# Optimization experiments

Measured on AMD Instinct MI355X. Metric: run time of the kernel, lower is better.

## Reference

```python
import jax, jax.numpy as jnp
import numpy as np

TEMPERATURE = 0.07
NORMALIZE = True
NEG_INF = -1e30


def setup_inputs() -> dict:
    key = jax.random.key(0)
    features = jax.random.normal(key, (8192, 512), dtype=jnp.float32)
    return {"features": features}


def reference(features):
    # features: [B, D]
    B = features.shape[0]
    if NORMALIZE:
        norm = jnp.linalg.norm(features, axis=1, keepdims=True)
        features = features / jnp.maximum(norm, 1e-12)
    # [B, B] similarity matrix
    sim = jnp.matmul(features, features.T) / TEMPERATURE

    # default SimCLR labels: arange(B//2) repeated twice -> pair (i, i + B//2)
    half = jnp.arange(B // 2, dtype=jnp.int32)
    labels = jnp.concatenate([half, half])
    eq = labels[None, :] == labels[:, None]          # [B, B]
    diag = jnp.eye(B, dtype=bool)
    mask_pos = eq & ~diag                            # positives per row

    # Original per-row CE: logits = cat(pos_sims, neg_sims) (= all j != i),
    # target index 0 = FIRST positive (lowest column index). Loss_i =
    # logsumexp_{j != i}(sim[i, j]) - sim[i, first_pos_i].
    sim_masked = jnp.where(diag, NEG_INF, sim)
    lse = jax.scipy.special.logsumexp(sim_masked, axis=1)   # [B]

    first_pos = jnp.argmax(mask_pos, axis=1)                 # first True per row
    pos_sim = jnp.take_along_axis(sim, first_pos[:, None], axis=1)[:, 0]

    has_pos = jnp.any(mask_pos, axis=1)
    losses = jnp.where(has_pos, lse - pos_sim, 0.0)
    count = jnp.maximum(jnp.sum(has_pos.astype(jnp.float32)), 1.0)
    return jnp.sum(losses) / count
```

## Files before the change

kernel.cpp:

```cpp
#include <hip/hip_runtime.h>
#include <hip/hip_bf16.h>
#include <stdint.h>

#define BATCH 8192
#define DIM   512
#define BM    256
#define BK    64
#define NT    (BATCH / BM)
#define NPAIR (NT * (NT + 1) / 2)

#define FEAT_SCALE 4.5398164f
#define LN2        0.69314718055994531f

typedef __attribute__((ext_vector_type(8))) short short8;
typedef __attribute__((ext_vector_type(4))) float f32x4;

__device__ __forceinline__ void gld_lds16(const void* g, void* l) {
  __builtin_amdgcn_global_load_lds(
      (__attribute__((address_space(1))) void*)(uintptr_t)g,
      (__attribute__((address_space(3))) void*)(uintptr_t)l,
      16, 0, 0);
}

__global__ __launch_bounds__(256) void normalize_bf16(
    const float* __restrict__ x, __hip_bfloat16* __restrict__ o,
    float* __restrict__ rowsum) {
  const int wv = threadIdx.x >> 6, lane = threadIdx.x & 63;
  const int row = blockIdx.x * 4 + wv;
  if (lane == 0) rowsum[row] = 0.0f;
  const float4* xr = (const float4*)(x + (size_t)row * DIM);
  const float4 v0 = xr[lane];
  const float4 v1 = xr[lane + 64];
  float ss = v0.x * v0.x + v0.y * v0.y + v0.z * v0.z + v0.w * v0.w +
             v1.x * v1.x + v1.y * v1.y + v1.z * v1.z + v1.w * v1.w;
#pragma unroll
  for (int m = 32; m > 0; m >>= 1) ss += __shfl_xor(ss, m, 64);
  const float inv = FEAT_SCALE / fmaxf(sqrtf(ss), 1e-12f);
  ushort4 p0, p1;
  p0.x = __bfloat16_as_ushort(__float2bfloat16(v0.x * inv));
  p0.y = __bfloat16_as_ushort(__float2bfloat16(v0.y * inv));
  p0.z = __bfloat16_as_ushort(__float2bfloat16(v0.z * inv));
  p0.w = __bfloat16_as_ushort(__float2bfloat16(v0.w * inv));
  p1.x = __bfloat16_as_ushort(__float2bfloat16(v1.x * inv));
  p1.y = __bfloat16_as_ushort(__float2bfloat16(v1.y * inv));
  p1.z = __bfloat16_as_ushort(__float2bfloat16(v1.z * inv));
  p1.w = __bfloat16_as_ushort(__float2bfloat16(v1.w * inv));
  ushort4* orow = (ushort4*)(o + (size_t)row * DIM);
  orow[lane]      = p0;
  orow[lane + 64] = p1;
}

__global__ __launch_bounds__(512, 2) void sim_lse_kernel(
    const __hip_bfloat16* __restrict__ F, float* __restrict__ rowsum,
    float* __restrict__ possim) {
  extern __shared__ char smem[];
  float* colAcc = (float*)(smem + 131072);

  const int t = blockIdx.x;
  int by = (int)((65.0f - sqrtf(65.0f * 65.0f - 8.0f * (float)t)) * 0.5f);
  if (by > NT - 1) by = NT - 1;
  if (by < 0) by = 0;
  while ((by + 1) * (65 - (by + 1)) / 2 <= t) ++by;
  while (by * (65 - by) / 2 > t) --by;
  const int bx = by + (t - by * (65 - by) / 2);
  const bool diagTile = (bx == by);
  const bool hasPos = (bx == by + NT / 2);

  const int rowBase = by * BM;
  const int colBase = bx * BM;

  const int tid  = threadIdx.x;
  const int lane = tid & 63;
  const int wv   = tid >> 6;
  const int q    = lane >> 4;
  const int l15  = lane & 15;
  const int waveM = wv >> 2;
  const int waveN = wv & 3;

  const int r0 = tid >> 2, s0 = tid & 3;
  const int r1 = (tid + 512) >> 2;
  const __hip_bfloat16* gA0 = F + (size_t)(rowBase + r0) * DIM + (s0 ^ (r0 & 3)) * 8;
  const __hip_bfloat16* gA1 = F + (size_t)(rowBase + r1) * DIM + (s0 ^ (r1 & 3)) * 8;
  const __hip_bfloat16* gB0 = F + (size_t)(colBase + r0) * DIM + (s0 ^ (r0 & 3)) * 8;
  const __hip_bfloat16* gB1 = F + (size_t)(colBase + r1) * DIM + (s0 ^ (r1 & 3)) * 8;
  char* ldsW0 = smem + wv * 1024;
  char* ldsW1 = ldsW0 + 8192;

  const int aoff = waveM * 8192 + l15 * 64 + ((q ^ (l15 & 3)) * 16);
  const int boff = waveN * 4096 + l15 * 64 + ((q ^ (l15 & 3)) * 16);
  const char* sA = smem;
  const char* sB = smem + 65536;

  if (tid < 256) colAcc[tid] = 0.0f;

  f32x4 acc[8][4] = {};
  short8 a[4], b0[4], b1[4];

#define BARRIER() asm volatile("s_barrier" ::: "memory")
#define VMCNT4()  asm volatile("s_waitcnt vmcnt(4)" ::: "memory")
#define SP1() __builtin_amdgcn_s_setprio(1)
#define SP0() __builtin_amdgcn_s_setprio(0)

#define STAGE(T_, KK_, ISB_) do {                                             \
    const __hip_bfloat16* g0_ = (ISB_) ? gB0 : gA0;                           \
    const __hip_bfloat16* g1_ = (ISB_) ? gB1 : gA1;                           \
    const int ko_ = ((T_) & 7) * BK + (KK_) * 32;                             \
    const int pl_ = ((((T_) & 1) * 2 + (KK_)) << 14) + ((ISB_) ? 65536 : 0);  \
    gld_lds16(g0_ + ko_, ldsW0 + pl_);                                        \
    gld_lds16(g1_ + ko_, ldsW1 + pl_);                                        \
  } while (0)

#define LDA4(PK_, H_) do {                                                    \
    const char* p_ = sA + ((PK_) << 14) + aoff + (H_) * 4096;                 \
    a[0] = *(const short8*)(p_);                                              \
    a[1] = *(const short8*)(p_ + 1024);                                       \
    a[2] = *(const short8*)(p_ + 2048);                                       \
    a[3] = *(const short8*)(p_ + 3072);                                       \
  } while (0)

#define LDB4(PK_, BV_) do {                                                   \
    const char* p_ = sB + ((PK_) << 14) + boff;                               \
    BV_[0] = *(const short8*)(p_);                                            \
    BV_[1] = *(const short8*)(p_ + 1024);                                     \
    BV_[2] = *(const short8*)(p_ + 2048);                                     \
    BV_[3] = *(const short8*)(p_ + 3072);                                     \
  } while (0)

#define MFMA16(H_, BV_) do {                                                  \
    _Pragma("unroll")                                                         \
    for (int m_ = 0; m_ < 4; ++m_)                                            \
      _Pragma("unroll")                                                       \
      for (int n_ = 0; n_ < 4; ++n_)                                          \
        acc[(H_) * 4 + m_][n_] = __builtin_amdgcn_mfma_f32_16x16x32_bf16(     \
            a[m_], BV_[n_], acc[(H_) * 4 + m_][n_], 0, 0, 0);                 \
  } while (0)

#define ITER(U_, V_) do {                                                     \
     LDA4(0, 0); LDB4(0, b0); STAGE((V_), 1, 0);                     \
    BARRIER(); SP1(); MFMA16(0, b0); SP0(); BARRIER();                        \
     LDA4(0, 1); STAGE((V_), 1, 1);                                  \
    BARRIER(); SP1(); MFMA16(1, b0); SP0(); BARRIER();                        \
     LDA4(1, 0); LDB4(1, b1); STAGE((U_) + 2, 0, 0);                 \
    BARRIER(); SP1(); MFMA16(0, b1); SP0(); BARRIER();                        \
     LDA4(1, 1); STAGE((U_) + 2, 0, 1); VMCNT4();                    \
    BARRIER(); SP1(); MFMA16(1, b1); SP0(); BARRIER();                        \
     LDA4(2, 0); LDB4(2, b0); STAGE((U_) + 2, 1, 0);                 \
    BARRIER(); SP1(); MFMA16(0, b0); SP0(); BARRIER();                        \
     LDA4(2, 1); STAGE((U_) + 2, 1, 1);                              \
    BARRIER(); SP1(); MFMA16(1, b0); SP0(); BARRIER();                        \
     LDA4(3, 0); LDB4(3, b1); STAGE((V_) + 2, 0, 0);                 \
    BARRIER(); SP1(); MFMA16(0, b1); SP0(); BARRIER();                        \
     LDA4(3, 1); STAGE((V_) + 2, 0, 1); VMCNT4();                    \
    BARRIER(); SP1(); MFMA16(1, b1); SP0(); BARRIER();                        \
  } while (0)

  STAGE(0, 0, 0); STAGE(0, 0, 1); STAGE(0, 1, 0); STAGE(0, 1, 1);
  STAGE(1, 0, 0); STAGE(1, 0, 1);
  asm volatile("s_waitcnt vmcnt(4) lgkmcnt(0)" ::: "memory");
  BARRIER();

  ITER(0, 1);
  ITER(2, 3);
  ITER(4, 5);
  ITER(6, 7);

  asm volatile("s_waitcnt vmcnt(0)" ::: "memory");
  BARRIER();

  float* redBuf = (float*)smem;
  float cp[4] = {0.f, 0.f, 0.f, 0.f};
  f32x4 rp[8];

#pragma unroll
  for (int mi = 0; mi < 8; ++mi) {
    f32x4 r = {0.f, 0.f, 0.f, 0.f};
#pragma unroll
    for (int ni = 0; ni < 4; ++ni) {
      const int lc = waveN * 64 + ni * 16 + l15;
#pragma unroll
      for (int rr = 0; rr < 4; ++rr) {
        const int lr = waveM * 128 + mi * 16 + q * 4 + rr;
        const float s = acc[mi][ni][rr];
        float e = exp2f(s);
        if (diagTile && lc == lr) e = 0.0f;
        r[rr] += e;
        cp[ni] += e;
        if (hasPos && lc == lr) {
          const int gi = rowBase + lr;
          possim[gi] = s;
          possim[gi + BATCH / 2] = s;
        }
      }
    }
    rp[mi] = r;
  }

  {
    float* wb = redBuf + (waveN * 16 + l15) * 260 + waveM * 128 + q * 4;
#pragma unroll
    for (int mi = 0; mi < 8; ++mi) *(f32x4*)(wb + mi * 16) = rp[mi];
  }

  if (!diagTile) {
#pragma unroll
    for (int ni = 0; ni < 4; ++ni) {
      float c = cp[ni];
      c += __shfl_xor(c, 16, 64);
      c += __shfl_xor(c, 32, 64);
      if (q == 0) atomicAdd(&colAcc[waveN * 64 + ni * 16 + l15], c);
    }
  }
  asm volatile("s_waitcnt lgkmcnt(0)" ::: "memory");
  BARRIER();

  {
    const int row = tid >> 1, half = tid & 1;
    const float* bp = redBuf + (half * 32) * 260 + row;
    float ssum = 0.f;
#pragma unroll
    for (int j = 0; j < 32; ++j) ssum += bp[j * 260];
    atomicAdd(&rowsum[rowBase + row], ssum);
  }
  if (!diagTile && tid < 256)
    atomicAdd(&rowsum[colBase + tid], colAcc[tid]);
}

__global__ __launch_bounds__(1024) void finalize_kernel(
    const float* __restrict__ rowsum, const float* __restrict__ possim,
    float* __restrict__ out) {
  float acc = 0.0f;
  for (int i = threadIdx.x; i < BATCH; i += 1024)
    acc += __logf(rowsum[i]) - possim[i] * LN2;
#pragma unroll
  for (int m = 32; m > 0; m >>= 1) acc += __shfl_xor(acc, m, 64);
  __shared__ float ws[16];
  const int lane = threadIdx.x & 63, wv = threadIdx.x >> 6;
  if (lane == 0) ws[wv] = acc;
  __syncthreads();
  if (threadIdx.x == 0) {
    float tot = 0.0f;
#pragma unroll
    for (int k = 0; k < 16; ++k) tot += ws[k];
    out[0] = tot * (1.0f / (float)BATCH);
  }
}

extern "C" void kernel_launch(void* const* d_in, const int* in_sizes, int n_in,
                              void* d_out, int out_size, void* d_ws, size_t ws_size,
                              hipStream_t stream) {
  const float* x = (const float*)d_in[0];
  float* out = (float*)d_out;

  __hip_bfloat16* Fb = (__hip_bfloat16*)d_ws;
  float* rowsum = (float*)((char*)d_ws + (size_t)BATCH * DIM * sizeof(__hip_bfloat16));
  float* possim = rowsum + BATCH;

  static bool attr_done = false;
  if (!attr_done) {
    (void)hipFuncSetAttribute(reinterpret_cast<const void*>(sim_lse_kernel),
                              hipFuncAttributeMaxDynamicSharedMemorySize, 132096);
    attr_done = true;
  }

  normalize_bf16<<<BATCH / 4, 256, 0, stream>>>(x, Fb, rowsum);
  sim_lse_kernel<<<NPAIR, 512, 132096, stream>>>(Fb, rowsum, possim);
  finalize_kernel<<<1, 1024, 0, stream>>>(rowsum, possim, out);
}
```

Baseline: 136.6 us.

## Split each 256x256 triangular tile into two 128x256 blocks with simpler pipeline

Each upper-triangular tile pair is now handled by two workgroups, each computing a 128-row by 256-column block. This halves the accumulator registers and cuts LDS to about 97KB, and it doubles the grid so more workgroups run at once for better occupancy and load balance. The K-loop is restructured into a uniform 16-phase pipeline with a new swizzle and a single B buffer per stage. The trade-off is that the column tile is loaded twice from global/L2, and the column-sum atomics double.

```diff
diff --git a/kernel.cpp b/kernel.cpp
--- a/kernel.cpp
+++ b/kernel.cpp
@@ -5,9 +5,9 @@
 #define BATCH 8192
 #define DIM   512
 #define BM    256
-#define BK    64
 #define NT    (BATCH / BM)
 #define NPAIR (NT * (NT + 1) / 2)
+#define NBLK  (NPAIR * 2)
 
 #define FEAT_SCALE 4.5398164f
 #define LN2        0.69314718055994531f
@@ -54,20 +54,22 @@
     const __hip_bfloat16* __restrict__ F, float* __restrict__ rowsum,
     float* __restrict__ possim) {
   extern __shared__ char smem[];
-  float* colAcc = (float*)(smem + 131072);
-
-  const int t = blockIdx.x;
-  int by = (int)((65.0f - sqrtf(65.0f * 65.0f - 8.0f * (float)t)) * 0.5f);
+  float* colAcc = (float*)(smem + 98304);
+
+  const int t  = blockIdx.x;
+  const int pr = t >> 1;
+  const int hb = t & 1;
+  int by = (int)((65.0f - sqrtf(65.0f * 65.0f - 8.0f * (float)pr)) * 0.5f);
   if (by > NT - 1) by = NT - 1;
   if (by < 0) by = 0;
-  while ((by + 1) * (65 - (by + 1)) / 2 <= t) ++by;
-  while (by * (65 - by) / 2 > t) --by;
-  const int bx = by + (t - by * (65 - by) / 2);
+  while ((by + 1) * (65 - (by + 1)) / 2 <= pr) ++by;
+  while (by * (65 - by) / 2 > pr) --by;
+  const int bx = by + (pr - by * (65 - by) / 2);
   const bool diagTile = (bx == by);
   const bool hasPos = (bx == by + NT / 2);
 
-  const int rowBase = by * BM;
-  const int colBase = bx * BM;
+  const int rowB = by * BM + hb * 128;
+  const int colB = bx * BM;
 
   const int tid  = threadIdx.x;
   const int lane = tid & 63;
@@ -77,116 +79,87 @@
   const int waveM = wv >> 2;
   const int waveN = wv & 3;
 
-  const int r0 = tid >> 2, s0 = tid & 3;
-  const int r1 = (tid + 512) >> 2;
-  const __hip_bfloat16* gA0 = F + (size_t)(rowBase + r0) * DIM + (s0 ^ (r0 & 3)) * 8;
-  const __hip_bfloat16* gA1 = F + (size_t)(rowBase + r1) * DIM + (s0 ^ (r1 & 3)) * 8;
-  const __hip_bfloat16* gB0 = F + (size_t)(colBase + r0) * DIM + (s0 ^ (r0 & 3)) * 8;
-  const __hip_bfloat16* gB1 = F + (size_t)(colBase + r1) * DIM + (s0 ^ (r1 & 3)) * 8;
-  char* ldsW0 = smem + wv * 1024;
-  char* ldsW1 = ldsW0 + 8192;
-
-  const int aoff = waveM * 8192 + l15 * 64 + ((q ^ (l15 & 3)) * 16);
-  const int boff = waveN * 4096 + l15 * 64 + ((q ^ (l15 & 3)) * 16);
-  const char* sA = smem;
-  const char* sB = smem + 65536;
+  const int rs = tid >> 2, ss = tid & 3;
+  const int sw = ss ^ ((rs >> 1) & 3);
+  const __hip_bfloat16* gA  = F + (size_t)(rowB + rs) * DIM + sw * 8;
+  const __hip_bfloat16* gB0 = F + (size_t)(colB + rs) * DIM + sw * 8;
+  const __hip_bfloat16* gB1 = gB0 + (size_t)128 * DIM;
+
+  const int swz  = (q ^ ((l15 >> 1) & 3)) * 16;
+  const int aoff = (waveM * 64 + l15) * 64 + swz;
+  const int boff = (waveN * 64 + l15) * 64 + swz;
 
   if (tid < 256) colAcc[tid] = 0.0f;
 
-  f32x4 acc[8][4] = {};
-  short8 a[4], b0[4], b1[4];
-
-#define BARRIER() asm volatile("s_barrier" ::: "memory")
-#define VMCNT4()  asm volatile("s_waitcnt vmcnt(4)" ::: "memory")
-#define SP1() __builtin_amdgcn_s_setprio(1)
-#define SP0() __builtin_amdgcn_s_setprio(0)
-
-#define STAGE(T_, KK_, ISB_) do {                                             \
-    const __hip_bfloat16* g0_ = (ISB_) ? gB0 : gA0;                           \
-    const __hip_bfloat16* g1_ = (ISB_) ? gB1 : gA1;                           \
-    const int ko_ = ((T_) & 7) * BK + (KK_) * 32;                             \
-    const int pl_ = ((((T_) & 1) * 2 + (KK_)) << 14) + ((ISB_) ? 65536 : 0);  \
-    gld_lds16(g0_ + ko_, ldsW0 + pl_);                                        \
-    gld_lds16(g1_ + ko_, ldsW1 + pl_);                                        \
+  f32x4 acc[4][4] = {};
+  short8 a[4], b[4];
+
+#define STAGE(T_, KK_) do {                                                   \
+    const int ko_ = ((T_) & 7) * 64 + (KK_) * 32;                             \
+    const int pb_ = ((T_) & 1) * 2 + (KK_);                                   \
+    gld_lds16(gA  + ko_, smem + pb_ * 8192 + wv * 1024);                      \
+    gld_lds16(gB0 + ko_, smem + 32768 + pb_ * 16384 + wv * 1024);             \
+    gld_lds16(gB1 + ko_, smem + 32768 + pb_ * 16384 + 8192 + wv * 1024);      \
   } while (0)
 
-#define LDA4(PK_, H_) do {                                                    \
-    const char* p_ = sA + ((PK_) << 14) + aoff + (H_) * 4096;                 \
-    a[0] = *(const short8*)(p_);                                              \
-    a[1] = *(const short8*)(p_ + 1024);                                       \
-    a[2] = *(const short8*)(p_ + 2048);                                       \
-    a[3] = *(const short8*)(p_ + 3072);                                       \
-  } while (0)
-
-#define LDB4(PK_, BV_) do {                                                   \
-    const char* p_ = sB + ((PK_) << 14) + boff;                               \
-    BV_[0] = *(const short8*)(p_);                                            \
-    BV_[1] = *(const short8*)(p_ + 1024);                                     \
-    BV_[2] = *(const short8*)(p_ + 2048);                                     \
-    BV_[3] = *(const short8*)(p_ + 3072);                                     \
-  } while (0)
-
-#define MFMA16(H_, BV_) do {                                                  \
+#define PHASE(TB_, KK_, ST_, SKK_) do {                                       \
+    const char* pa_ = smem + ((TB_) * 2 + (KK_)) * 8192 + aoff;               \
+    a[0] = *(const short8*)(pa_);                                             \
+    a[1] = *(const short8*)(pa_ + 1024);                                      \
+    a[2] = *(const short8*)(pa_ + 2048);                                      \
+    a[3] = *(const short8*)(pa_ + 3072);                                      \
+    const char* pb_ = smem + 32768 + ((TB_) * 2 + (KK_)) * 16384 + boff;      \
+    b[0] = *(const short8*)(pb_);                                             \
+    b[1] = *(const short8*)(pb_ + 1024);                                      \
+    b[2] = *(const short8*)(pb_ + 2048);                                      \
+    b[3] = *(const short8*)(pb_ + 3072);                                      \
+    STAGE(ST_, SKK_);                                                         \
+    asm volatile("s_waitcnt vmcnt(6)" ::: "memory");                          \
+    __builtin_amdgcn_s_barrier();                                             \
+    __builtin_amdgcn_s_setprio(1);                                            \
     _Pragma("unroll")                                                         \
     for (int m_ = 0; m_ < 4; ++m_)                                            \
       _Pragma("unroll")                                                       \
       for (int n_ = 0; n_ < 4; ++n_)                                          \
-        acc[(H_) * 4 + m_][n_] = __builtin_amdgcn_mfma_f32_16x16x32_bf16(     \
-            a[m_], BV_[n_], acc[(H_) * 4 + m_][n_], 0, 0, 0);                 \
+        acc[m_][n_] = __builtin_amdgcn_mfma_f32_16x16x32_bf16(                \
+            a[m_], b[n_], acc[m_][n_], 0, 0, 0);                              \
+    __builtin_amdgcn_s_setprio(0);                                            \
+    __builtin_amdgcn_s_barrier();                                             \
   } while (0)
 
-#define ITER(U_, V_) do {                                                     \
-     LDA4(0, 0); LDB4(0, b0); STAGE((V_), 1, 0);                     \
-    BARRIER(); SP1(); MFMA16(0, b0); SP0(); BARRIER();                        \
-     LDA4(0, 1); STAGE((V_), 1, 1);                                  \
-    BARRIER(); SP1(); MFMA16(1, b0); SP0(); BARRIER();                        \
-     LDA4(1, 0); LDB4(1, b1); STAGE((U_) + 2, 0, 0);                 \
-    BARRIER(); SP1(); MFMA16(0, b1); SP0(); BARRIER();                        \
-     LDA4(1, 1); STAGE((U_) + 2, 0, 1); VMCNT4();                    \
-    BARRIER(); SP1(); MFMA16(1, b1); SP0(); BARRIER();                        \
-     LDA4(2, 0); LDB4(2, b0); STAGE((U_) + 2, 1, 0);                 \
-    BARRIER(); SP1(); MFMA16(0, b0); SP0(); BARRIER();                        \
-     LDA4(2, 1); STAGE((U_) + 2, 1, 1);                              \
-    BARRIER(); SP1(); MFMA16(1, b0); SP0(); BARRIER();                        \
-     LDA4(3, 0); LDB4(3, b1); STAGE((V_) + 2, 0, 0);                 \
-    BARRIER(); SP1(); MFMA16(0, b1); SP0(); BARRIER();                        \
-     LDA4(3, 1); STAGE((V_) + 2, 0, 1); VMCNT4();                    \
-    BARRIER(); SP1(); MFMA16(1, b1); SP0(); BARRIER();                        \
-  } while (0)
-
-  STAGE(0, 0, 0); STAGE(0, 0, 1); STAGE(0, 1, 0); STAGE(0, 1, 1);
-  STAGE(1, 0, 0); STAGE(1, 0, 1);
-  asm volatile("s_waitcnt vmcnt(4) lgkmcnt(0)" ::: "memory");
-  BARRIER();
-
-  ITER(0, 1);
-  ITER(2, 3);
-  ITER(4, 5);
-  ITER(6, 7);
+  STAGE(0, 0); STAGE(0, 1); STAGE(1, 0);
+  asm volatile("s_waitcnt vmcnt(3)" ::: "memory");
+  __builtin_amdgcn_s_barrier();
+
+#pragma unroll
+  for (int T = 0; T < 8; ++T) {
+    PHASE(T & 1, 0, T + 1, 1);
+    PHASE(T & 1, 1, T + 2, 0);
+  }
 
   asm volatile("s_waitcnt vmcnt(0)" ::: "memory");
-  BARRIER();
+  __builtin_amdgcn_s_barrier();
 
   float* redBuf = (float*)smem;
   float cp[4] = {0.f, 0.f, 0.f, 0.f};
-  f32x4 rp[8];
-
-#pragma unroll
-  for (int mi = 0; mi < 8; ++mi) {
+  f32x4 rp[4];
+
+#pragma unroll
+  for (int mi = 0; mi < 4; ++mi) {
     f32x4 r = {0.f, 0.f, 0.f, 0.f};
 #pragma unroll
     for (int ni = 0; ni < 4; ++ni) {
       const int lc = waveN * 64 + ni * 16 + l15;
 #pragma unroll
       for (int rr = 0; rr < 4; ++rr) {
-        const int lr = waveM * 128 + mi * 16 + q * 4 + rr;
+        const int lr = waveM * 64 + mi * 16 + q * 4 + rr;
         const float s = acc[mi][ni][rr];
         float e = exp2f(s);
-        if (diagTile && lc == lr) e = 0.0f;
+        if (diagTile && lc == hb * 128 + lr) e = 0.0f;
         r[rr] += e;
         cp[ni] += e;
-        if (hasPos && lc == lr) {
-          const int gi = rowBase + lr;
+        if (hasPos && lc == hb * 128 + lr) {
+          const int gi = rowB + lr;
           possim[gi] = s;
           possim[gi + BATCH / 2] = s;
         }
@@ -196,9 +169,9 @@
   }
 
   {
-    float* wb = redBuf + (waveN * 16 + l15) * 260 + waveM * 128 + q * 4;
-#pragma unroll
-    for (int mi = 0; mi < 8; ++mi) *(f32x4*)(wb + mi * 16) = rp[mi];
+    float* wb = redBuf + (waveN * 16 + l15) * 132 + waveM * 64 + q * 4;
+#pragma unroll
+    for (int mi = 0; mi < 4; ++mi) *(f32x4*)(wb + mi * 16) = rp[mi];
   }
 
   if (!diagTile) {
@@ -211,18 +184,20 @@
     }
   }
   asm volatile("s_waitcnt lgkmcnt(0)" ::: "memory");
-  BARRIER();
+  __builtin_amdgcn_s_barrier();
 
   {
-    const int row = tid >> 1, half = tid & 1;
-    const float* bp = redBuf + (half * 32) * 260 + row;
-    float ssum = 0.f;
-#pragma unroll
-    for (int j = 0; j < 32; ++j) ssum += bp[j * 260];
-    atomicAdd(&rowsum[rowBase + row], ssum);
+    const int row = tid >> 2, g = tid & 3;
+    const float* bp = redBuf + g * 132 + row;
+    float s = 0.f;
+#pragma unroll
+    for (int j = 0; j < 16; ++j) s += bp[j * 528];
+    s += __shfl_xor(s, 1, 64);
+    s += __shfl_xor(s, 2, 64);
+    if (g == 0) atomicAdd(&rowsum[rowB + row], s);
   }
   if (!diagTile && tid < 256)
-    atomicAdd(&rowsum[colBase + tid], colAcc[tid]);
+    atomicAdd(&rowsum[colB + tid], colAcc[tid]);
 }
 
 __global__ __launch_bounds__(1024) void finalize_kernel(
@@ -258,11 +233,11 @@
   static bool attr_done = false;
   if (!attr_done) {
     (void)hipFuncSetAttribute(reinterpret_cast<const void*>(sim_lse_kernel),
-                              hipFuncAttributeMaxDynamicSharedMemorySize, 132096);
+                              hipFuncAttributeMaxDynamicSharedMemorySize, 99328);
     attr_done = true;
   }
 
   normalize_bf16<<<BATCH / 4, 256, 0, stream>>>(x, Fb, rowsum);
-  sim_lse_kernel<<<NPAIR, 512, 132096, stream>>>(Fb, rowsum, possim);
+  sim_lse_kernel<<<NBLK, 512, 99328, stream>>>(Fb, rowsum, possim);
   finalize_kernel<<<1, 1024, 0, stream>>>(rowsum, possim, out);
 }
```

Measured after the change: 128.4 us. 1.06x faster.
